# Performance work log

Hardware: AMD Instinct MI355X
Metric: run time of the kernel (lower is better)

The kernel has to match this reference:

```python
import jax, jax.numpy as jnp
import numpy as np
from jax import lax

B, C, H, WIN, K = 8, 128, 128, 4, 3
WS = H // 2           # window_size = input_resolution / sqrt(win_num)
L = H * H
DN = ('NCHW', 'OIHW', 'NCHW')


def setup_inputs() -> dict:
    key = jax.random.key(0)
    ks = jax.random.split(key, 12)
    s = 0.02
    return {
        'x': jax.random.normal(ks[0], (B, L, C), jnp.float32),
        # ConvLayer1 params: (win_num*dim, dim, k, k), grouped conv, no bias
        'conv1_w': jax.random.normal(ks[1], (WIN * C, C, K, K), jnp.float32) * s,
        'dc_w': jax.random.normal(ks[2], (WIN, C), jnp.float32) * s,
        'dc_b': jax.random.normal(ks[3], (WIN,), jnp.float32) * s,
        'l1_w': jax.random.normal(ks[4], (4 * WIN, WIN), jnp.float32) * s,
        'l1_b': jax.random.normal(ks[5], (4 * WIN,), jnp.float32) * s,
        'l2_w': jax.random.normal(ks[6], (WIN, 4 * WIN), jnp.float32) * s,
        'l2_b': jax.random.normal(ks[7], (WIN,), jnp.float32) * s,
        'gk_w': jax.random.normal(ks[8], (C, WIN, C), jnp.float32) * s,
        'gk_b': jax.random.normal(ks[9], (C,), jnp.float32) * s,
        'fusion_w': jax.random.normal(ks[10], (C, (WIN + 1) * C), jnp.float32) * s,
        'fusion_b': jax.random.normal(ks[11], (C,), jnp.float32) * s,
    }


def reference(x, conv1_w, dc_w, dc_b, l1_w, l1_b, l2_w, l2_b, gk_w, gk_b, fusion_w, fusion_b):
    Bx = x.shape[0]
    # ka_window_partition: (B, L, C) -> (B, win_num*C, WS, WS), window-major channels
    xw = x.reshape(Bx, 2, WS, 2, WS, C).transpose(0, 1, 3, 5, 2, 4).reshape(Bx, WIN * C, WS, WS)
    # convlayer1: grouped conv, groups=win_num
    wc1 = lax.conv_general_dilated(xw, conv1_w, (1, 1), [(1, 1), (1, 1)],
                                   feature_group_count=WIN, dimension_numbers=DN)
    # SE-style window reweighting
    pooled = wc1.mean(axis=(2, 3)).reshape(Bx, WIN, C)          # adaptive avg pool
    ww = jnp.einsum('bwc,wc->bw', pooled, dc_w) + dc_b          # grouped 1x1 downchannel
    ww = jax.nn.gelu(ww @ l1_w.T + l1_b, approximate=False)
    ww = jax.nn.sigmoid(ww @ l2_w.T + l2_b)
    kern = ww[:, :, None, None, None, None] * conv1_w.reshape(WIN, C, C, K, K)[None]
    gk = jnp.einsum('owj,bwijhk->biohk', gk_w, kern) + gk_b[None, None, :, None, None]
    allk = jnp.concatenate([kern, gk[:, None]], axis=1)
    w_all = allk.reshape(Bx * (WIN + 1) * C, C, K, K)
    ximg = x.reshape(Bx, H, H, C).transpose(0, 3, 1, 2)
    xrep = jnp.tile(ximg, (1, WIN + 1, 1, 1)).reshape(1, Bx * (WIN + 1) * C, H, H)
    y = lax.conv_general_dilated(xrep, w_all, (1, 1), [(1, 1), (1, 1)],
                                 feature_group_count=Bx * (WIN + 1), dimension_numbers=DN)
    y = y.reshape(Bx, (WIN + 1) * C, H, H)
    out = jnp.einsum('oc,bchw->bohw', fusion_w, y) + fusion_b[None, :, None, None]
    return out.transpose(0, 2, 3, 1).reshape(Bx, L, C)
```

## Files before the change

### kernel.cpp

```cpp
#include <hip/hip_runtime.h>
#include <hip/hip_bf16.h>
#include <cmath>

typedef unsigned short u16;
typedef __attribute__((ext_vector_type(8))) short bf16x8;
typedef __attribute__((ext_vector_type(4))) float f32x4;
typedef __attribute__((ext_vector_type(4))) unsigned short u16x4;

#define OFF_AGG   0u
#define OFF_WW    81920u
#define OFF_R     82048u
#define OFF_FSUM  100480u
#define OFF_GKT   100992u
#define OFF_A     363136u
#define OFF_P     2722432u
#define OFF_M     5081728u
#define OFF_KEFF  7441024u
#define OFF_XPAD  9800320u

__device__ __forceinline__ u16 f2bf(float f) {
  union { float f; unsigned int u; } v; v.f = f;
  unsigned int r = v.u + 0x7FFFu + ((v.u >> 16) & 1u);
  return (u16)(r >> 16);
}

__global__ void kw(const float* __restrict__ dc_w, const float* __restrict__ conv1_w,
                   const float* __restrict__ gk_w, const float* __restrict__ fusion_w,
                   float* __restrict__ R, float* __restrict__ gkT,
                   float* __restrict__ fsum, float* __restrict__ agg,
                   float* __restrict__ A, float* __restrict__ P) {
  const int bid = blockIdx.x, tid = threadIdx.x;
  if (bid < 18) {
    int gid = bid * 256 + tid;
    int w = gid / 1152, m = gid % 1152;
    float s = 0.f;
    for (int o = 0; o < 128; ++o)
      s += dc_w[w * 128 + o] * conv1_w[(size_t)(w * 128 + o) * 1152 + m];
    R[gid] = s;
  } else if (bid < 274) {
    int gid = (bid - 18) * 256 + tid;
    int w = gid >> 14, j = (gid >> 7) & 127, c = gid & 127;
    gkT[gid] = gk_w[c * 512 + w * 128 + j];
  } else if (bid == 274) {
    if (tid < 128) {
      float s = 0.f;
      for (int oc = 0; oc < 128; ++oc) s += fusion_w[tid * 640 + 512 + oc];
      fsum[tid] = s;
    }
  } else if (bid < 279) {
    const int idx = (bid - 275) * 256 + tid;
    f32x4 z = {0.f, 0.f, 0.f, 0.f};
    #pragma unroll
    for (int k = 0; k < 5; ++k)
      *(f32x4*)(agg + idx * 20 + k * 4) = z;
  } else {
    int gid = (bid - 279) * 256 + tid;
    int w = gid / 36864;
    int rem = gid % 36864;
    int o = rem / 288;
    int m = (rem % 288) * 4;
    const float* fw1 = fusion_w + o * 640 + w * 128;
    const float* fw4 = fusion_w + o * 640 + 512;
    const float* cw = conv1_w + (size_t)w * 128 * 1152 + m;
    float a0 = 0, a1 = 0, a2 = 0, a3 = 0, p0 = 0, p1 = 0, p2 = 0, p3 = 0;
    for (int oc = 0; oc < 128; ++oc) {
      float f1 = fw1[oc], f4 = fw4[oc];
      float4 cv = *(const float4*)(cw + (size_t)oc * 1152);
      a0 += f1 * cv.x; a1 += f1 * cv.y; a2 += f1 * cv.z; a3 += f1 * cv.w;
      p0 += f4 * cv.x; p1 += f4 * cv.y; p2 += f4 * cv.z; p3 += f4 * cv.w;
    }
    float4* Ao = (float4*)(A + (size_t)(w * 128 + o) * 1152 + m);
    float4* Po = (float4*)(P + (size_t)(w * 128 + o) * 1152 + m);
    *Ao = make_float4(a0, a1, a2, a3);
    *Po = make_float4(p0, p1, p2, p3);
  }
}

__global__ void k1_pad_agg(const float* __restrict__ x, u16* __restrict__ xpad,
                           float* __restrict__ agg) {
  const int rp = blockIdx.x;
  const int b = blockIdx.y;
  const int tid = threadIdx.x;
  const size_t xpb = ((size_t)b * 130 + rp) * 16640;
  if (rp == 0 || rp == 129) {
    const bf16x8 z = {0, 0, 0, 0, 0, 0, 0, 0};
    #pragma unroll
    for (int rr = 0; rr < 8; ++rr)
      *(bf16x8*)(xpad + xpb + (size_t)(rr * 256 + tid) * 8) = z;
    if (tid < 32)
      *(bf16x8*)(xpad + xpb + (size_t)(2048 + tid) * 8) = z;
    return;
  }
  const int r = rp - 1;
  if (tid < 32) {
    *(u16x4*)(xpad + xpb + tid * 4) = (u16x4){0, 0, 0, 0};
  } else if (tid < 64) {
    *(u16x4*)(xpad + xpb + 129 * 128 + (tid - 32) * 4) = (u16x4){0, 0, 0, 0};
  }
  const int s = tid >> 5;
  const int cg = tid & 31;
  const int c0 = cg * 4;
  const float* xr = x + ((size_t)b * 16384 + (size_t)r * 128) * 128;
  f32x4 sum = {0.f, 0.f, 0.f, 0.f};
  f32x4 cap = {0.f, 0.f, 0.f, 0.f};
  #pragma unroll
  for (int qi = 0; qi < 16; ++qi) {
    const int q = s * 16 + qi;
    f32x4 v = *(const f32x4*)(xr + (size_t)q * 128 + c0);
    sum += v;
    if (qi == 0 && (s == 0 || s == 4)) cap = v;
    if (qi == 15 && (s == 3 || s == 7)) cap = v;
    u16x4 st = { f2bf(v[0]), f2bf(v[1]), f2bf(v[2]), f2bf(v[3]) };
    *(u16x4*)(xpad + xpb + (size_t)(q + 1) * 128 + c0) = st;
  }
  const int i = r >> 6, rw = r & 63;
  const int abase = b * 512 + c0;
  if (s == 0) {
    #pragma unroll
    for (int k = 0; k < 4; ++k) atomicAdd(&agg[3 * 4096 + abase + (i * 2) * 128 + k], cap[k]);
  } else if (s == 4) {
    #pragma unroll
    for (int k = 0; k < 4; ++k) atomicAdd(&agg[3 * 4096 + abase + (i * 2 + 1) * 128 + k], cap[k]);
  } else if (s == 3) {
    #pragma unroll
    for (int k = 0; k < 4; ++k) atomicAdd(&agg[4 * 4096 + abase + (i * 2) * 128 + k], cap[k]);
  } else if (s == 7) {
    #pragma unroll
    for (int k = 0; k < 4; ++k) atomicAdd(&agg[4 * 4096 + abase + (i * 2 + 1) * 128 + k], cap[k]);
  }
  __shared__ f32x4 ls[8][32];
  ls[s][cg] = sum;
  __syncthreads();
  if (tid < 64) {
    const int h = tid >> 5, g = tid & 31;
    f32x4 T = ls[h * 4 + 0][g] + ls[h * 4 + 1][g] + ls[h * 4 + 2][g] + ls[h * 4 + 3][g];
    const int a = b * 512 + (i * 2 + h) * 128 + g * 4;
    #pragma unroll
    for (int k = 0; k < 4; ++k) atomicAdd(&agg[a + k], T[k]);
    if (rw == 0) {
      #pragma unroll
      for (int k = 0; k < 4; ++k) atomicAdd(&agg[4096 + a + k], T[k]);
    }
    if (rw == 63) {
      #pragma unroll
      for (int k = 0; k < 4; ++k) atomicAdd(&agg[2 * 4096 + a + k], T[k]);
    }
  }
}

__global__ void k2_ww(const float* __restrict__ x, const float* __restrict__ agg,
                      const float* __restrict__ R, const float* __restrict__ dc_b,
                      const float* __restrict__ l1_w, const float* __restrict__ l1_b,
                      const float* __restrict__ l2_w, const float* __restrict__ l2_b,
                      float* __restrict__ ww) {
  const int b = blockIdx.x;
  const int tid = threadIdx.x;
  const int w = tid >> 6, lane = tid & 63;
  __shared__ float red[4];
  float partial = 0.f;
  const int i = w >> 1, j = w & 1;
  const int r0 = i * 64, s0 = j * 64;
  const size_t base = (size_t)b * 16384 * 128;
  #pragma unroll
  for (int k = 0; k < 2; ++k) {
    const int c = lane * 2 + k;
    const int ai = b * 512 + w * 128 + c;
    float T  = agg[ai];
    float rF = agg[4096 + ai];
    float rL = agg[2 * 4096 + ai];
    float cF = agg[3 * 4096 + ai];
    float cL = agg[4 * 4096 + ai];
    float c00 = x[base + ((size_t)(r0 + 0)  * 128 + (s0 + 0))  * 128 + c];
    float c0L = x[base + ((size_t)(r0 + 0)  * 128 + (s0 + 63)) * 128 + c];
    float cL0 = x[base + ((size_t)(r0 + 63) * 128 + (s0 + 0))  * 128 + c];
    float cLL = x[base + ((size_t)(r0 + 63) * 128 + (s0 + 63)) * 128 + c];
    float S[9];
    S[0] = T - rL - cL + cLL;
    S[1] = T - rL;
    S[2] = T - rL - cF + cL0;
    S[3] = T - cL;
    S[4] = T;
    S[5] = T - cF;
    S[6] = T - rF - cL + c0L;
    S[7] = T - rF;
    S[8] = T - rF - cF + c00;
    const float* Rp = R + (w * 128 + c) * 9;
    #pragma unroll
    for (int t = 0; t < 9; ++t) partial += S[t] * Rp[t];
  }
  for (int off = 32; off > 0; off >>= 1) partial += __shfl_xor(partial, off, 64);
  if (lane == 0) red[w] = partial;
  __syncthreads();
  if (tid == 0) {
    float ww0[4];
    #pragma unroll
    for (int w2 = 0; w2 < 4; ++w2) ww0[w2] = red[w2] * (1.f / 4096.f) + dc_b[w2];
    float h1[16];
    for (int i2 = 0; i2 < 16; ++i2) {
      float s = l1_b[i2];
      #pragma unroll
      for (int w2 = 0; w2 < 4; ++w2) s += l1_w[i2 * 4 + w2] * ww0[w2];
      h1[i2] = 0.5f * s * (1.f + erff(s * 0.70710678118654752f));
    }
    for (int w2 = 0; w2 < 4; ++w2) {
      float s = l2_b[w2];
      for (int i2 = 0; i2 < 16; ++i2) s += l2_w[w2 * 16 + i2] * h1[i2];
      ww[b * 4 + w2] = 1.f / (1.f + expf(-s));
    }
  }
}

__global__ void k45_keff(const float* __restrict__ A, const float* __restrict__ P,
                         const float* __restrict__ gkT, const float* __restrict__ ww,
                         const float* __restrict__ fsum, const float* __restrict__ gk_b,
                         u16* __restrict__ keff) {
  const int t = blockIdx.x >> 6;
  const int o0 = (blockIdx.x & 63) * 2;
  const int tid = threadIdx.x;
  __shared__ float pl[2][4][128];
  __shared__ float al[2][4][128];
  __shared__ float red[2][2][4][128];
  #pragma unroll
  for (int rr = 0; rr < 4; ++rr) {
    const int idx = rr * 256 + tid;
    const int oi = idx >> 9, w = (idx >> 7) & 3, j = idx & 127;
    const size_t src = (size_t)(w * 128 + o0 + oi) * 1152 + j * 9 + t;
    pl[oi][w][j] = P[src];
    al[oi][w][j] = A[src];
  }
  __syncthreads();
  const int c = tid & 127, jh = tid >> 7;
  float acc[2][4];
  #pragma unroll
  for (int oi = 0; oi < 2; ++oi)
    #pragma unroll
    for (int w = 0; w < 4; ++w) acc[oi][w] = 0.f;
  const float* g = gkT + c;
  #pragma unroll 4
  for (int j = jh * 64; j < jh * 64 + 64; ++j) {
    const float g0 = g[0 * 16384 + j * 128];
    const float g1 = g[1 * 16384 + j * 128];
    const float g2 = g[2 * 16384 + j * 128];
    const float g3 = g[3 * 16384 + j * 128];
    #pragma unroll
    for (int oi = 0; oi < 2; ++oi) {
      acc[oi][0] += pl[oi][0][j] * g0;
      acc[oi][1] += pl[oi][1][j] * g1;
      acc[oi][2] += pl[oi][2][j] * g2;
      acc[oi][3] += pl[oi][3][j] * g3;
    }
  }
  #pragma unroll
  for (int oi = 0; oi < 2; ++oi)
    #pragma unroll
    for (int w = 0; w < 4; ++w) red[jh][oi][w][c] = acc[oi][w];
  __syncthreads();
  const int oi2 = tid >> 7, c2 = tid & 127;
  float m[4];
  #pragma unroll
  for (int w = 0; w < 4; ++w)
    m[w] = red[0][oi2][w][c2] + red[1][oi2][w][c2] + al[oi2][w][c2];
  const float base = fsum[o0 + oi2] * gk_b[c2];
  #pragma unroll
  for (int b = 0; b < 8; ++b) {
    float r = base;
    #pragma unroll
    for (int w = 0; w < 4; ++w) r += ww[b * 4 + w] * m[w];
    keff[(size_t)b * 147456 + (size_t)t * 16384 + (o0 + oi2) * 128 + c2] = f2bf(r);
  }
}

__global__ __launch_bounds__(256, 2) void k6_conv(
    const u16* __restrict__ xpad, const u16* __restrict__ keff,
    const float* __restrict__ fusion_b, float* __restrict__ out) {
  __shared__ __align__(16) u16 alds[130 * 128];
  __shared__ __align__(16) u16 apad[256];
  __shared__ __align__(16) u16 wlds[128 * 128];
  const int tid = threadIdx.x;
  const int blk = blockIdx.x;
  const int b = blk & 7;
  const int p = blk >> 3;
  const int wid = tid >> 6;
  const int lane = tid & 63;
  const int wm = (wid & 1) * 64;
  const int wn = (wid >> 1) * 64;
  const int quad = lane >> 4;
  const int l16 = lane & 15;

  f32x4 acc[4][4];
  #pragma unroll
  for (int i = 0; i < 4; ++i)
    #pragma unroll
    for (int j = 0; j < 4; ++j)
      acc[i][j] = (f32x4){0.f, 0.f, 0.f, 0.f};

  const u16* kb = keff + (size_t)b * 147456;
  const u16* xb = xpad + (size_t)b * 130 * 16640;
  bf16x8 streg[8];
  (void)apad;

  auto stage_W_load = [&](int tap) {
    const u16* src = kb + tap * 16384;
    #pragma unroll
    for (int it = 0; it < 8; ++it) {
      const int chunk = it * 256 + tid;
      const int gs = chunk ^ ((chunk >> 4) & 7);
      streg[it] = *(const bf16x8*)(src + gs * 8);
    }
  };
  auto stage_W_write = [&]() {
    #pragma unroll
    for (int it = 0; it < 8; ++it)
      *(bf16x8*)(wlds + (it * 256 + tid) * 8) = streg[it];
  };
  auto stage_A_dma = [&](int prow) {
    const u16* src = xb + (size_t)prow * 16640;
    #pragma unroll
    for (int r = 0; r < 8; ++r) {
      const int chunk = (wid * 8 + r) * 64 + lane;
      const int gs = chunk ^ ((chunk >> 4) & 7);
      __builtin_amdgcn_global_load_lds(
          (const __attribute__((address_space(1))) unsigned int*)(src + (size_t)gs * 8),
          (__attribute__((address_space(3))) unsigned int*)(alds + (wid * 8 + r) * 512),
          16, 0, 0);
    }
    if (tid < 32) {
      const int chunk = 2048 + tid;
      const int gs = chunk ^ ((chunk >> 4) & 7);
      __builtin_amdgcn_global_load_lds(
          (const __attribute__((address_space(1))) unsigned int*)(src + (size_t)gs * 8),
          (__attribute__((address_space(3))) unsigned int*)(alds + 2048 * 8),
          16, 0, 0);
    }
  };

  stage_W_load(0);
  stage_A_dma(p);
  stage_W_write();
  __syncthreads();

  for (int tap = 0; tap < 9; ++tap) {
    if (tap < 8) stage_W_load(tap + 1);
    const int dw = tap % 3 - 1;
    const int pixoff = 1 + dw;
    #pragma unroll
    for (int kc = 0; kc < 4; ++kc) {
      const int c0 = kc * 32 + quad * 8;
      bf16x8 a[4], bb[4];
      #pragma unroll
      for (int i = 0; i < 4; ++i) {
        const int pix = pixoff + wm + i * 16 + l16;
        const int off = (pix * 128 + c0) ^ ((pix & 7) << 3);
        a[i] = *(const bf16x8*)(alds + off);
      }
      #pragma unroll
      for (int j = 0; j < 4; ++j) {
        const int row = wn + j * 16 + l16;
        const int off = (row * 128 + c0) ^ ((row & 7) << 3);
        bb[j] = *(const bf16x8*)(wlds + off);
      }
      #pragma unroll
      for (int i = 0; i < 4; ++i)
        #pragma unroll
        for (int j = 0; j < 4; ++j)
          acc[i][j] = __builtin_amdgcn_mfma_f32_16x16x32_bf16(a[i], bb[j], acc[i][j], 0, 0, 0);
    }
    __syncthreads();
    if (tap < 8) {
      if (tap % 3 == 2) stage_A_dma(p + (tap + 1) / 3);
      stage_W_write();
      __syncthreads();
    }
  }

  float fb[4];
  #pragma unroll
  for (int j = 0; j < 4; ++j) fb[j] = fusion_b[wn + j * 16 + l16];
  float* outb = out + ((size_t)b * 16384 + (size_t)p * 128) * 128;
  #pragma unroll
  for (int i = 0; i < 4; ++i)
    #pragma unroll
    for (int r = 0; r < 4; ++r) {
      const int m = wm + i * 16 + quad * 4 + r;
      #pragma unroll
      for (int j = 0; j < 4; ++j)
        outb[(size_t)m * 128 + (wn + j * 16 + l16)] = acc[i][j][r] + fb[j];
    }
}

extern "C" void kernel_launch(void* const* d_in, const int* in_sizes, int n_in,
                              void* d_out, int out_size, void* d_ws, size_t ws_size,
                              hipStream_t stream) {
  const float* x        = (const float*)d_in[0];
  const float* conv1_w  = (const float*)d_in[1];
  const float* dc_w     = (const float*)d_in[2];
  const float* dc_b     = (const float*)d_in[3];
  const float* l1_w     = (const float*)d_in[4];
  const float* l1_b     = (const float*)d_in[5];
  const float* l2_w     = (const float*)d_in[6];
  const float* l2_b     = (const float*)d_in[7];
  const float* gk_w     = (const float*)d_in[8];
  const float* gk_b     = (const float*)d_in[9];
  const float* fusion_w = (const float*)d_in[10];
  const float* fusion_b = (const float*)d_in[11];
  float* out = (float*)d_out;
  char* ws = (char*)d_ws;

  float* agg  = (float*)(ws + OFF_AGG);
  float* wwp  = (float*)(ws + OFF_WW);
  float* R    = (float*)(ws + OFF_R);
  float* fsum = (float*)(ws + OFF_FSUM);
  float* gkT  = (float*)(ws + OFF_GKT);
  float* A    = (float*)(ws + OFF_A);
  float* P    = (float*)(ws + OFF_P);
  u16* keff   = (u16*)(ws + OFF_KEFF);
  u16* xpad   = (u16*)(ws + OFF_XPAD);

  kw<<<855, 256, 0, stream>>>(dc_w, conv1_w, gk_w, fusion_w, R, gkT, fsum, agg, A, P);
  k1_pad_agg<<<dim3(130, 8), 256, 0, stream>>>(x, xpad, agg);
  k2_ww<<<8, 256, 0, stream>>>(x, agg, R, dc_b, l1_w, l1_b, l2_w, l2_b, wwp);
  k45_keff<<<576, 256, 0, stream>>>(A, P, gkT, wwp, fsum, gk_b, keff);
  k6_conv<<<1024, 256, 0, stream>>>(xpad, keff, fusion_b, out);
}
```

Measured before the change: 226.7 us.

## Merge weight-prep and pad/aggregate kernels, replace atomics with per-row partial buffers

Merges the weight preprocessing kernel and the x padding/aggregation kernel into a single launch. The atomic accumulation into agg is replaced by per-row partial sums (rowT, colF, colL), which k2_ww then reduces itself, so the agg zeroing pass and its atomics go away. The conv kernel also issues the W staging write before the A DMA. The cost is that k2_ww, running on only 8 blocks, now performs a 64-row serial reduction, and colL aliases the keff buffer, which is safe only because keff is written after k2 finishes.

```diff
diff --git a/kernel.cpp b/kernel.cpp
--- a/kernel.cpp
+++ b/kernel.cpp
@@ -24,12 +24,16 @@
   return (u16)(r >> 16);
 }
 
-__global__ void kw(const float* __restrict__ dc_w, const float* __restrict__ conv1_w,
-                   const float* __restrict__ gk_w, const float* __restrict__ fusion_w,
-                   float* __restrict__ R, float* __restrict__ gkT,
-                   float* __restrict__ fsum, float* __restrict__ agg,
-                   float* __restrict__ A, float* __restrict__ P) {
+__global__ void kd1(const float* __restrict__ dc_w, const float* __restrict__ conv1_w,
+                    const float* __restrict__ gk_w, const float* __restrict__ fusion_w,
+                    const float* __restrict__ x,
+                    float* __restrict__ R, float* __restrict__ gkT,
+                    float* __restrict__ fsum, float* __restrict__ A,
+                    float* __restrict__ P, u16* __restrict__ xpad,
+                    float* __restrict__ rowT, float* __restrict__ colF,
+                    float* __restrict__ colL) {
   const int bid = blockIdx.x, tid = threadIdx.x;
+  __shared__ f32x4 ls[8][32];
   if (bid < 18) {
     int gid = bid * 256 + tid;
     int w = gid / 1152, m = gid % 1152;
@@ -47,14 +51,8 @@
       for (int oc = 0; oc < 128; ++oc) s += fusion_w[tid * 640 + 512 + oc];
       fsum[tid] = s;
     }
-  } else if (bid < 279) {
-    const int idx = (bid - 275) * 256 + tid;
-    f32x4 z = {0.f, 0.f, 0.f, 0.f};
-    #pragma unroll
-    for (int k = 0; k < 5; ++k)
-      *(f32x4*)(agg + idx * 20 + k * 4) = z;
-  } else {
-    int gid = (bid - 279) * 256 + tid;
+  } else if (bid < 851) {
+    int gid = (bid - 275) * 256 + tid;
     int w = gid / 36864;
     int rem = gid % 36864;
     int o = rem / 288;
@@ -73,83 +71,60 @@
     float4* Po = (float4*)(P + (size_t)(w * 128 + o) * 1152 + m);
     *Ao = make_float4(a0, a1, a2, a3);
     *Po = make_float4(p0, p1, p2, p3);
-  }
-}
-
-__global__ void k1_pad_agg(const float* __restrict__ x, u16* __restrict__ xpad,
-                           float* __restrict__ agg) {
-  const int rp = blockIdx.x;
-  const int b = blockIdx.y;
-  const int tid = threadIdx.x;
-  const size_t xpb = ((size_t)b * 130 + rp) * 16640;
-  if (rp == 0 || rp == 129) {
-    const bf16x8 z = {0, 0, 0, 0, 0, 0, 0, 0};
-    #pragma unroll
-    for (int rr = 0; rr < 8; ++rr)
-      *(bf16x8*)(xpad + xpb + (size_t)(rr * 256 + tid) * 8) = z;
-    if (tid < 32)
-      *(bf16x8*)(xpad + xpb + (size_t)(2048 + tid) * 8) = z;
-    return;
-  }
-  const int r = rp - 1;
-  if (tid < 32) {
-    *(u16x4*)(xpad + xpb + tid * 4) = (u16x4){0, 0, 0, 0};
-  } else if (tid < 64) {
-    *(u16x4*)(xpad + xpb + 129 * 128 + (tid - 32) * 4) = (u16x4){0, 0, 0, 0};
-  }
-  const int s = tid >> 5;
-  const int cg = tid & 31;
-  const int c0 = cg * 4;
-  const float* xr = x + ((size_t)b * 16384 + (size_t)r * 128) * 128;
-  f32x4 sum = {0.f, 0.f, 0.f, 0.f};
-  f32x4 cap = {0.f, 0.f, 0.f, 0.f};
-  #pragma unroll
-  for (int qi = 0; qi < 16; ++qi) {
-    const int q = s * 16 + qi;
-    f32x4 v = *(const f32x4*)(xr + (size_t)q * 128 + c0);
-    sum += v;
-    if (qi == 0 && (s == 0 || s == 4)) cap = v;
-    if (qi == 15 && (s == 3 || s == 7)) cap = v;
-    u16x4 st = { f2bf(v[0]), f2bf(v[1]), f2bf(v[2]), f2bf(v[3]) };
-    *(u16x4*)(xpad + xpb + (size_t)(q + 1) * 128 + c0) = st;
-  }
-  const int i = r >> 6, rw = r & 63;
-  const int abase = b * 512 + c0;
-  if (s == 0) {
-    #pragma unroll
-    for (int k = 0; k < 4; ++k) atomicAdd(&agg[3 * 4096 + abase + (i * 2) * 128 + k], cap[k]);
-  } else if (s == 4) {
-    #pragma unroll
-    for (int k = 0; k < 4; ++k) atomicAdd(&agg[3 * 4096 + abase + (i * 2 + 1) * 128 + k], cap[k]);
-  } else if (s == 3) {
-    #pragma unroll
-    for (int k = 0; k < 4; ++k) atomicAdd(&agg[4 * 4096 + abase + (i * 2) * 128 + k], cap[k]);
-  } else if (s == 7) {
-    #pragma unroll
-    for (int k = 0; k < 4; ++k) atomicAdd(&agg[4 * 4096 + abase + (i * 2 + 1) * 128 + k], cap[k]);
-  }
-  __shared__ f32x4 ls[8][32];
-  ls[s][cg] = sum;
-  __syncthreads();
-  if (tid < 64) {
-    const int h = tid >> 5, g = tid & 31;
-    f32x4 T = ls[h * 4 + 0][g] + ls[h * 4 + 1][g] + ls[h * 4 + 2][g] + ls[h * 4 + 3][g];
-    const int a = b * 512 + (i * 2 + h) * 128 + g * 4;
-    #pragma unroll
-    for (int k = 0; k < 4; ++k) atomicAdd(&agg[a + k], T[k]);
-    if (rw == 0) {
-      #pragma unroll
-      for (int k = 0; k < 4; ++k) atomicAdd(&agg[4096 + a + k], T[k]);
-    }
-    if (rw == 63) {
-      #pragma unroll
-      for (int k = 0; k < 4; ++k) atomicAdd(&agg[2 * 4096 + a + k], T[k]);
-    }
-  }
-}
-
-__global__ void k2_ww(const float* __restrict__ x, const float* __restrict__ agg,
-                      const float* __restrict__ R, const float* __restrict__ dc_b,
+  } else {
+    const int kb = bid - 851;
+    const int rp = kb % 130;
+    const int b = kb / 130;
+    const size_t xpb = ((size_t)b * 130 + rp) * 16640;
+    if (rp == 0 || rp == 129) {
+      const bf16x8 z = {0, 0, 0, 0, 0, 0, 0, 0};
+      #pragma unroll
+      for (int rr = 0; rr < 8; ++rr)
+        *(bf16x8*)(xpad + xpb + (size_t)(rr * 256 + tid) * 8) = z;
+      if (tid < 32)
+        *(bf16x8*)(xpad + xpb + (size_t)(2048 + tid) * 8) = z;
+      return;
+    }
+    const int r = rp - 1;
+    if (tid < 32) {
+      *(u16x4*)(xpad + xpb + tid * 4) = (u16x4){0, 0, 0, 0};
+    } else if (tid < 64) {
+      *(u16x4*)(xpad + xpb + 129 * 128 + (tid - 32) * 4) = (u16x4){0, 0, 0, 0};
+    }
+    const int s = tid >> 5;
+    const int cg = tid & 31;
+    const int c0 = cg * 4;
+    const float* xr = x + ((size_t)b * 16384 + (size_t)r * 128) * 128;
+    f32x4 sum = {0.f, 0.f, 0.f, 0.f};
+    f32x4 cap = {0.f, 0.f, 0.f, 0.f};
+    #pragma unroll
+    for (int qi = 0; qi < 16; ++qi) {
+      const int q = s * 16 + qi;
+      f32x4 v = *(const f32x4*)(xr + (size_t)q * 128 + c0);
+      sum += v;
+      if (qi == 0 && (s == 0 || s == 4)) cap = v;
+      if (qi == 15 && (s == 3 || s == 7)) cap = v;
+      u16x4 st = { f2bf(v[0]), f2bf(v[1]), f2bf(v[2]), f2bf(v[3]) };
+      *(u16x4*)(xpad + xpb + (size_t)(q + 1) * 128 + c0) = st;
+    }
+    const size_t rT2 = ((size_t)b * 128 + r) * 2;
+    if (s == 0)      *(f32x4*)(colF + (rT2 + 0) * 128 + c0) = cap;
+    else if (s == 4) *(f32x4*)(colF + (rT2 + 1) * 128 + c0) = cap;
+    else if (s == 3) *(f32x4*)(colL + (rT2 + 0) * 128 + c0) = cap;
+    else if (s == 7) *(f32x4*)(colL + (rT2 + 1) * 128 + c0) = cap;
+    ls[s][cg] = sum;
+    __syncthreads();
+    if (tid < 64) {
+      const int h = tid >> 5, g = tid & 31;
+      f32x4 T = ls[h * 4 + 0][g] + ls[h * 4 + 1][g] + ls[h * 4 + 2][g] + ls[h * 4 + 3][g];
+      *(f32x4*)(rowT + (rT2 + h) * 128 + g * 4) = T;
+    }
+  }
+}
+
+__global__ void k2_ww(const float* __restrict__ rowT, const float* __restrict__ colF,
+                      const float* __restrict__ colL, const float* __restrict__ R,
+                      const float* __restrict__ dc_b,
                       const float* __restrict__ l1_w, const float* __restrict__ l1_b,
                       const float* __restrict__ l2_w, const float* __restrict__ l2_b,
                       float* __restrict__ ww) {
@@ -157,23 +132,25 @@
   const int tid = threadIdx.x;
   const int w = tid >> 6, lane = tid & 63;
   __shared__ float red[4];
+  const int i = w >> 1, j = w & 1;
   float partial = 0.f;
-  const int i = w >> 1, j = w & 1;
-  const int r0 = i * 64, s0 = j * 64;
-  const size_t base = (size_t)b * 16384 * 128;
   #pragma unroll
   for (int k = 0; k < 2; ++k) {
     const int c = lane * 2 + k;
-    const int ai = b * 512 + w * 128 + c;
-    float T  = agg[ai];
-    float rF = agg[4096 + ai];
-    float rL = agg[2 * 4096 + ai];
-    float cF = agg[3 * 4096 + ai];
-    float cL = agg[4 * 4096 + ai];
-    float c00 = x[base + ((size_t)(r0 + 0)  * 128 + (s0 + 0))  * 128 + c];
-    float c0L = x[base + ((size_t)(r0 + 0)  * 128 + (s0 + 63)) * 128 + c];
-    float cL0 = x[base + ((size_t)(r0 + 63) * 128 + (s0 + 0))  * 128 + c];
-    float cLL = x[base + ((size_t)(r0 + 63) * 128 + (s0 + 63)) * 128 + c];
+    const size_t rbase = ((size_t)b * 128 + i * 64) * 2 + j;
+    float T = 0.f, cF = 0.f, cL = 0.f;
+    #pragma unroll 4
+    for (int ri = 0; ri < 64; ++ri) {
+      const size_t idx = (rbase + (size_t)ri * 2) * 128 + c;
+      T  += rowT[idx];
+      cF += colF[idx];
+      cL += colL[idx];
+    }
+    const size_t i0 = rbase * 128 + c;
+    const size_t i63 = (rbase + 126) * 128 + c;
+    const float rF = rowT[i0], rL = rowT[i63];
+    const float c00 = colF[i0], c0L = colL[i0];
+    const float cL0 = colF[i63], cLL = colL[i63];
     float S[9];
     S[0] = T - rL - cL + cLL;
     S[1] = T - rL;
@@ -367,8 +344,8 @@
     }
     __syncthreads();
     if (tap < 8) {
+      stage_W_write();
       if (tap % 3 == 2) stage_A_dma(p + (tap + 1) / 3);
-      stage_W_write();
       __syncthreads();
     }
   }
@@ -406,19 +383,21 @@
   float* out = (float*)d_out;
   char* ws = (char*)d_ws;
 
-  float* agg  = (float*)(ws + OFF_AGG);
   float* wwp  = (float*)(ws + OFF_WW);
   float* R    = (float*)(ws + OFF_R);
   float* fsum = (float*)(ws + OFF_FSUM);
   float* gkT  = (float*)(ws + OFF_GKT);
   float* A    = (float*)(ws + OFF_A);
   float* P    = (float*)(ws + OFF_P);
+  float* rowT = (float*)(ws + OFF_M);
+  float* colF = (float*)(ws + OFF_M + 1048576u);
+  float* colL = (float*)(ws + OFF_KEFF);
   u16* keff   = (u16*)(ws + OFF_KEFF);
   u16* xpad   = (u16*)(ws + OFF_XPAD);
 
-  kw<<<855, 256, 0, stream>>>(dc_w, conv1_w, gk_w, fusion_w, R, gkT, fsum, agg, A, P);
-  k1_pad_agg<<<dim3(130, 8), 256, 0, stream>>>(x, xpad, agg);
-  k2_ww<<<8, 256, 0, stream>>>(x, agg, R, dc_b, l1_w, l1_b, l2_w, l2_b, wwp);
+  kd1<<<1891, 256, 0, stream>>>(dc_w, conv1_w, gk_w, fusion_w, x,
+                                R, gkT, fsum, A, P, xpad, rowT, colF, colL);
+  k2_ww<<<8, 256, 0, stream>>>(rowT, colF, colL, R, dc_b, l1_w, l1_b, l2_w, l2_b, wwp);
   k45_keff<<<576, 256, 0, stream>>>(A, P, gkT, wwp, fsum, gk_b, keff);
   k6_conv<<<1024, 256, 0, stream>>>(xpad, keff, fusion_b, out);
 }
```

Result: faster. 219.0 us (-3.4%).
